# Optimization experiments

Measured on AMD Instinct MI355X. Metric: run time of the kernel, lower is better.

The kernel has to match this reference:

```python
import jax, jax.numpy as jnp
import numpy as np

N = 4096      # n_nodes
IN = 256      # in_features
H = 4         # n_heads
F = 64        # out_features (per head)
SLOPE = 0.2   # leaky relu negative slope


def setup_inputs() -> dict:
    key = jax.random.key(0)
    k0, k1, k2, k3 = jax.random.split(key, 4)
    h = jax.random.normal(k0, (N, IN), dtype=jnp.float32)
    adj = jax.random.randint(k1, (N, N), 0, 2, dtype=jnp.int32)
    # ensure every node has at least one neighbor (self-loop) so softmax is defined
    adj = jnp.maximum(adj, jnp.eye(N, dtype=jnp.int32))
    # linear: in_features -> out_features * n_heads (xavier-ish scale)
    W = jax.random.normal(k2, (H * F, IN), dtype=jnp.float32) * np.float32(1.0 / np.sqrt(IN))
    b = jnp.zeros((H * F,), dtype=jnp.float32)
    # attn: Linear(2*F -> 1), weight row vector of size 2F plus scalar bias
    attn_w = jax.random.normal(k3, (2 * F,), dtype=jnp.float32) * np.float32(1.0 / np.sqrt(2 * F))
    attn_b = jnp.zeros((1,), dtype=jnp.float32)
    return {"h": h, "adj_mat": adj, "W": W, "b": b, "attn_w": attn_w, "attn_b": attn_b}


def reference(h, adj_mat, W, b, attn_w, attn_b):
    n = h.shape[0]
    # node projection: [N, H, F]
    g = (h @ W.T + b).reshape(n, H, F)
    # attn(concat(h_i, h_j)) = <a_src, g_i> + <a_dst, g_j> + bias  (decomposed, same math)
    src = jnp.einsum('nhf,f->nh', g, attn_w[:F])   # [N, H] contribution of node i
    dst = jnp.einsum('nhf,f->nh', g, attn_w[F:])   # [N, H] contribution of node j
    e = src[:, None, :] + dst[None, :, :] + attn_b[0]   # [N, N, H]
    e = jnp.where(e >= 0, e, SLOPE * e)                 # leaky relu
    e = jnp.where(adj_mat[:, :, None] != 0, e, -jnp.inf)  # mask non-edges
    a = jax.nn.softmax(e, axis=1)                       # softmax over neighbors j
    out = jnp.einsum('ijh,jhf->ihf', a, g)              # [N, H, F]
    return out.mean(axis=1)                             # average heads -> [N, F]
```

## Files before the change

kernel.cpp:

```cpp
#include <hip/hip_runtime.h>
#include <stdint.h>

constexpr int NODES = 4096;
constexpr int KIN   = 256;
constexpr int NHEAD = 4;
constexpr int NF    = 64;
constexpr int HFQ   = 256;
#define SLOPE 0.2f
#define L2E 1.44269504088896340736f

typedef __attribute__((ext_vector_type(8))) short short8;
typedef __attribute__((ext_vector_type(4))) float floatx4;
typedef __attribute__((ext_vector_type(16))) float f32x16;

static __device__ __forceinline__ unsigned short f2bf(float f) {
  return __builtin_bit_cast(unsigned short, (__bf16)f);
}

__global__ __launch_bounds__(256) void pack_prep_kernel(
    const int* __restrict__ adj, unsigned* __restrict__ bm,
    const float* __restrict__ hin, const float* __restrict__ Win,
    unsigned short* __restrict__ hB, unsigned short* __restrict__ WB) {
  int tid = threadIdx.x;
  if (blockIdx.x < 2048) {
    int wv = blockIdx.x * 4 + (tid >> 6);
    int lane = tid & 63;
    int jw = wv & 127;
    int it = wv >> 7;
    int i = it * 64 + lane;
    const int4* p = reinterpret_cast<const int4*>(adj + (size_t)i * NODES + jw * 32);
    unsigned m = 0;
#pragma unroll
    for (int q = 0; q < 8; ++q) {
      int4 a = p[q];
      m |= (a.x != 0 ? 1u : 0u) << (q * 4);
      m |= (a.y != 0 ? 1u : 0u) << (q * 4 + 1);
      m |= (a.z != 0 ? 1u : 0u) << (q * 4 + 2);
      m |= (a.w != 0 ? 1u : 0u) << (q * 4 + 3);
    }
    bm[(size_t)jw * NODES + i] = m;
  } else {
    int idx = (blockIdx.x - 2048) * 256 + tid;
    const int NH4 = (NODES * KIN) / 4;
    const int NW4 = (HFQ * KIN) / 4;
    if (idx < NH4) {
      float4 v = reinterpret_cast<const float4*>(hin)[idx];
      ushort4 o = { f2bf(v.x), f2bf(v.y), f2bf(v.z), f2bf(v.w) };
      reinterpret_cast<ushort4*>(hB)[idx] = o;
    } else if (idx < NH4 + NW4) {
      int j = idx - NH4;
      float4 v = reinterpret_cast<const float4*>(Win)[j];
      ushort4 o = { f2bf(v.x), f2bf(v.y), f2bf(v.z), f2bf(v.w) };
      reinterpret_cast<ushort4*>(WB)[j] = o;
    }
  }
}

__global__ __launch_bounds__(256) void proj_kernel(
    const unsigned short* __restrict__ hB, const unsigned short* __restrict__ WB,
    const float* __restrict__ bias,
    float* __restrict__ g32, unsigned short* __restrict__ gT3) {
  int wave = threadIdx.x >> 6, lane = threadIdx.x & 63;
  int tile = blockIdx.x * 4 + wave;
  int mt = tile >> 4, nt = tile & 15;
  int m0 = mt * 16, n0 = nt * 16;
  int r = lane & 15, kg = lane >> 4;
  floatx4 acc = {0.f, 0.f, 0.f, 0.f};
  const short8* Ap = reinterpret_cast<const short8*>(hB + (m0 + r) * KIN + kg * 8);
  const short8* Bp = reinterpret_cast<const short8*>(WB + (n0 + r) * KIN + kg * 8);
#pragma unroll
  for (int kb = 0; kb < 8; ++kb) {
    short8 a = Ap[kb * 4];
    short8 b = Bp[kb * 4];
    acc = __builtin_amdgcn_mfma_f32_16x16x32_bf16(a, b, acc, 0, 0, 0);
  }
  int col = n0 + r;
  float bv = bias[col];
  int head = col >> 6, half = (col >> 5) & 1, il = col & 31;
#pragma unroll
  for (int q = 0; q < 4; ++q) {
    int row = m0 + kg * 4 + q;
    float v = acc[q] + bv;
    g32[row * HFQ + col] = v;
    int si = (row >> 5) * 8192 + head * 2048 + half * 1024 +
             ((row >> 4) & 1) * 512 + ((row >> 3) & 1) * 256 + il * 8 + (row & 7);
    gT3[si] = f2bf(v);
  }
}

__global__ __launch_bounds__(256) void srcdst_kernel(
    const float* __restrict__ g32, const float* __restrict__ attn_w,
    const float* __restrict__ attn_b,
    float4* __restrict__ srcP, unsigned* __restrict__ eP) {
  int wave = threadIdx.x >> 6, lane = threadIdx.x & 63;
  int n = blockIdx.x * 4 + wave;
  float aws = attn_w[lane], awd = attn_w[64 + lane];
  float ab = attn_b[0];
#pragma unroll
  for (int hh = 0; hh < NHEAD; ++hh) {
    float v = g32[n * HFQ + hh * NF + lane];
    float s = v * aws, d = v * awd;
#pragma unroll
    for (int m = 32; m >= 1; m >>= 1) {
      s += __shfl_xor(s, m, 64);
      d += __shfl_xor(d, m, 64);
    }
    if (lane == 0) {
      s += ab;
      float4 sp;
      sp.x = exp2f(s * L2E);
      sp.y = exp2f(0.2f * s * L2E);
      sp.z = exp2f(-s * L2E);
      sp.w = 0.f;
      srcP[n * NHEAD + hh] = sp;
      float e1 = exp2f(d * L2E), e2 = exp2f(0.2f * d * L2E);
      eP[hh * NODES + n] = ((unsigned)f2bf(e2) << 16) | (unsigned)f2bf(e1);
    }
  }
}

__global__ __launch_bounds__(256, 4) void attn_kernel(
    const unsigned* __restrict__ bm, const unsigned short* __restrict__ gT3,
    const float4* __restrict__ srcP, const unsigned* __restrict__ eP,
    float* __restrict__ pnum, float* __restrict__ pden, int JP) {
  int tid = threadIdx.x;
  int hh = tid >> 6, lane = tid & 63;
  int il = lane & 31, hi = lane >> 5;
  int part = blockIdx.x, itile = blockIdx.y;
  int jstart = part * JP;
  int i = itile * 32 + il;

  float4 sp = srcP[i * NHEAD + hh];
  float es1 = sp.x, es2 = sp.y, thr = sp.z;

  f32x16 acc0 = {0.f,0.f,0.f,0.f,0.f,0.f,0.f,0.f,0.f,0.f,0.f,0.f,0.f,0.f,0.f,0.f};
  f32x16 acc1 = acc0, accd = acc0;

  short8 ones;
#pragma unroll
  for (int r = 0; r < 8; ++r) ones[r] = (short)0x3F80;

  const unsigned* epb = eP + hh * NODES;
  const unsigned short* Ab = gT3 + hh * 2048;

  int nsteps = JP / 32;
  for (int stp = 0; stp < nsteps; ++stp) {
    int j0 = jstart + stp * 32;
    unsigned mwd = bm[(size_t)(j0 >> 5) * NODES + i];
    const unsigned short* At = Ab + (size_t)(j0 >> 5) * 8192;
#pragma unroll
    for (int ch = 0; ch < 2; ++ch) {
      int jc = j0 + ch * 16 + hi * 8;
      uint4 ea = *reinterpret_cast<const uint4*>(epb + jc);
      uint4 eb = *reinterpret_cast<const uint4*>(epb + jc + 4);
      unsigned mb = (mwd >> (ch * 16 + hi * 8)) & 0xFFu;
      unsigned ev[8] = {ea.x, ea.y, ea.z, ea.w, eb.x, eb.y, eb.z, eb.w};
      short8 bfr;
#pragma unroll
      for (int r = 0; r < 8; ++r) {
        float e1f = __builtin_bit_cast(float, ev[r] << 16);
        float e2f = __builtin_bit_cast(float, ev[r] & 0xFFFF0000u);
        bool sel = e1f >= thr;
        float w = (sel ? es1 : es2) * (sel ? e1f : e2f);
        w = (mb & (1u << r)) ? w : 0.f;
        bfr[r] = (short)f2bf(w);
      }
      const short8 a0 = *reinterpret_cast<const short8*>(At + ch * 512 + hi * 256 + il * 8);
      const short8 a1 = *reinterpret_cast<const short8*>(At + 1024 + ch * 512 + hi * 256 + il * 8);
      acc0 = __builtin_amdgcn_mfma_f32_32x32x16_bf16(a0, bfr, acc0, 0, 0, 0);
      acc1 = __builtin_amdgcn_mfma_f32_32x32x16_bf16(a1, bfr, acc1, 0, 0, 0);
      accd = __builtin_amdgcn_mfma_f32_32x32x16_bf16(ones, bfr, accd, 0, 0, 0);
    }
  }

  if (hi == 0)
    pden[(size_t)part * (NODES * NHEAD) + i * NHEAD + hh] = accd[0];

  float* pbase = pnum + (size_t)part * (NODES * HFQ) + (size_t)i * HFQ + hh * NF;
#pragma unroll
  for (int reg = 0; reg < 16; ++reg) {
    int crow = (reg & 3) + 8 * (reg >> 2) + 4 * hi;
    pbase[crow] = acc0[reg];
    pbase[32 + crow] = acc1[reg];
  }
}

__global__ __launch_bounds__(256) void combine_kernel(
    const float* __restrict__ pnum, const float* __restrict__ pden,
    float* __restrict__ out, int NP) {
  int idx = blockIdx.x * 256 + threadIdx.x;
  int i = idx >> 6, f = idx & 63;
  float o = 0.f;
#pragma unroll
  for (int hh = 0; hh < NHEAD; ++hh) {
    float num = 0.f, den = 0.f;
    for (int p = 0; p < NP; ++p) {
      num += pnum[p * (NODES * HFQ) + i * HFQ + hh * NF + f];
      den += pden[p * (NODES * NHEAD) + i * NHEAD + hh];
    }
    o += num / den;
  }
  out[idx] = 0.25f * o;
}

extern "C" void kernel_launch(void* const* d_in, const int* in_sizes, int n_in,
                              void* d_out, int out_size, void* d_ws, size_t ws_size,
                              hipStream_t stream) {
  const float* hin = (const float*)d_in[0];
  const int* adj   = (const int*)d_in[1];
  const float* W   = (const float*)d_in[2];
  const float* b   = (const float*)d_in[3];
  const float* aw  = (const float*)d_in[4];
  const float* ab  = (const float*)d_in[5];
  float* out = (float*)d_out;
  char* ws = (char*)d_ws;

  unsigned short* hB  = (unsigned short*)(ws + 0x000000);
  unsigned short* WB  = (unsigned short*)(ws + 0x200000);
  float* g32          = (float*)(ws + 0x400000);
  unsigned short* gT3 = (unsigned short*)(ws + 0x800000);
  float4* srcP        = (float4*)(ws + 0xA00000);
  unsigned* eP        = (unsigned*)(ws + 0xA40000);
  unsigned* bm        = (unsigned*)(ws + 0xA60000);
  float* pden         = (float*)(ws + 0xC60000);
  float* pnum         = (float*)(ws + 0xD00000);
  const size_t base = 0xD00000;

  int NP = 2;
  if (ws_size >= base + 8ull * NODES * HFQ * 4) NP = 8;
  else if (ws_size >= base + 4ull * NODES * HFQ * 4) NP = 4;
  int JP = NODES / NP;

  pack_prep_kernel<<<2048 + 1088, 256, 0, stream>>>(adj, bm, hin, W, hB, WB);
  proj_kernel<<<1024, 256, 0, stream>>>(hB, WB, b, g32, gT3);
  srcdst_kernel<<<1024, 256, 0, stream>>>(g32, aw, ab, srcP, eP);
  attn_kernel<<<dim3(NP, 128), 256, 0, stream>>>(bm, gT3, srcP, eP, pnum, pden, JP);
  combine_kernel<<<1024, 256, 0, stream>>>(pnum, pden, out, NP);
}
```

Baseline: 82.18 us.

## Switch attention aggregation to 16x16x32 MFMA tiles with 16-node row tiles

The attention kernel now uses 16x16x32 bf16 MFMAs over 16 destination nodes per block instead of 32x32x16 over 32 nodes. The grid doubles along the node axis and the launch bound allows 8 blocks per CU. The projection kernel's bf16 transposed-g layout is rearranged to match the new fragment layout. The aim is higher occupancy and more parallel blocks through smaller accumulators. In exchange, each block recomputes the per-edge weight work for fewer outputs, the ones-vector denominator MFMA is a larger share of the work, and the bf16 g tiles are reloaded by twice as many blocks.

```diff
diff --git a/kernel.cpp b/kernel.cpp
--- a/kernel.cpp
+++ b/kernel.cpp
@@ -11,7 +11,6 @@
 
 typedef __attribute__((ext_vector_type(8))) short short8;
 typedef __attribute__((ext_vector_type(4))) float floatx4;
-typedef __attribute__((ext_vector_type(16))) float f32x16;
 
 static __device__ __forceinline__ unsigned short f2bf(float f) {
   return __builtin_bit_cast(unsigned short, (__bf16)f);
@@ -76,14 +75,14 @@
   }
   int col = n0 + r;
   float bv = bias[col];
-  int head = col >> 6, half = (col >> 5) & 1, il = col & 31;
+  int head = col >> 6, ct = (col & 63) >> 4, c15 = col & 15;
 #pragma unroll
   for (int q = 0; q < 4; ++q) {
     int row = m0 + kg * 4 + q;
     float v = acc[q] + bv;
     g32[row * HFQ + col] = v;
-    int si = (row >> 5) * 8192 + head * 2048 + half * 1024 +
-             ((row >> 4) & 1) * 512 + ((row >> 3) & 1) * 256 + il * 8 + (row & 7);
+    int si = (row >> 5) * 8192 + head * 2048 + ct * 512 +
+             (((row >> 3) & 3) * 16 + c15) * 8 + (row & 7);
     gT3[si] = f2bf(v);
   }
 }
@@ -119,22 +118,22 @@
   }
 }
 
-__global__ __launch_bounds__(256, 4) void attn_kernel(
+__global__ __launch_bounds__(256, 8) void attn_kernel(
     const unsigned* __restrict__ bm, const unsigned short* __restrict__ gT3,
     const float4* __restrict__ srcP, const unsigned* __restrict__ eP,
     float* __restrict__ pnum, float* __restrict__ pden, int JP) {
   int tid = threadIdx.x;
   int hh = tid >> 6, lane = tid & 63;
-  int il = lane & 31, hi = lane >> 5;
+  int il = lane & 15, kg = lane >> 4;
   int part = blockIdx.x, itile = blockIdx.y;
   int jstart = part * JP;
-  int i = itile * 32 + il;
+  int i = itile * 16 + il;
 
   float4 sp = srcP[i * NHEAD + hh];
   float es1 = sp.x, es2 = sp.y, thr = sp.z;
 
-  f32x16 acc0 = {0.f,0.f,0.f,0.f,0.f,0.f,0.f,0.f,0.f,0.f,0.f,0.f,0.f,0.f,0.f,0.f};
-  f32x16 acc1 = acc0, accd = acc0;
+  floatx4 acc0 = {0.f, 0.f, 0.f, 0.f};
+  floatx4 acc1 = acc0, acc2 = acc0, acc3 = acc0, accd = acc0;
 
   short8 ones;
 #pragma unroll
@@ -146,42 +145,46 @@
   int nsteps = JP / 32;
   for (int stp = 0; stp < nsteps; ++stp) {
     int j0 = jstart + stp * 32;
-    unsigned mwd = bm[(size_t)(j0 >> 5) * NODES + i];
-    const unsigned short* At = Ab + (size_t)(j0 >> 5) * 8192;
-#pragma unroll
-    for (int ch = 0; ch < 2; ++ch) {
-      int jc = j0 + ch * 16 + hi * 8;
-      uint4 ea = *reinterpret_cast<const uint4*>(epb + jc);
-      uint4 eb = *reinterpret_cast<const uint4*>(epb + jc + 4);
-      unsigned mb = (mwd >> (ch * 16 + hi * 8)) & 0xFFu;
-      unsigned ev[8] = {ea.x, ea.y, ea.z, ea.w, eb.x, eb.y, eb.z, eb.w};
-      short8 bfr;
-#pragma unroll
-      for (int r = 0; r < 8; ++r) {
-        float e1f = __builtin_bit_cast(float, ev[r] << 16);
-        float e2f = __builtin_bit_cast(float, ev[r] & 0xFFFF0000u);
-        bool sel = e1f >= thr;
-        float w = (sel ? es1 : es2) * (sel ? e1f : e2f);
-        w = (mb & (1u << r)) ? w : 0.f;
-        bfr[r] = (short)f2bf(w);
-      }
-      const short8 a0 = *reinterpret_cast<const short8*>(At + ch * 512 + hi * 256 + il * 8);
-      const short8 a1 = *reinterpret_cast<const short8*>(At + 1024 + ch * 512 + hi * 256 + il * 8);
-      acc0 = __builtin_amdgcn_mfma_f32_32x32x16_bf16(a0, bfr, acc0, 0, 0, 0);
-      acc1 = __builtin_amdgcn_mfma_f32_32x32x16_bf16(a1, bfr, acc1, 0, 0, 0);
-      accd = __builtin_amdgcn_mfma_f32_32x32x16_bf16(ones, bfr, accd, 0, 0, 0);
-    }
-  }
-
-  if (hi == 0)
+    int jt = j0 >> 5;
+    unsigned mwd = bm[(size_t)jt * NODES + i];
+    unsigned mb = (mwd >> (kg * 8)) & 0xFFu;
+    const unsigned* ep = epb + j0 + kg * 8;
+    uint4 ea = *reinterpret_cast<const uint4*>(ep);
+    uint4 eb = *reinterpret_cast<const uint4*>(ep + 4);
+    unsigned ev[8] = {ea.x, ea.y, ea.z, ea.w, eb.x, eb.y, eb.z, eb.w};
+    short8 bfr;
+#pragma unroll
+    for (int r = 0; r < 8; ++r) {
+      float e1f = __builtin_bit_cast(float, ev[r] << 16);
+      float e2f = __builtin_bit_cast(float, ev[r] & 0xFFFF0000u);
+      bool sel = e1f >= thr;
+      float w = (sel ? es1 : es2) * (sel ? e1f : e2f);
+      w = (mb & (1u << r)) ? w : 0.f;
+      bfr[r] = (short)f2bf(w);
+    }
+    const unsigned short* At = Ab + (size_t)jt * 8192;
+    const short8 a0 = *reinterpret_cast<const short8*>(At + 0 * 512 + lane * 8);
+    const short8 a1 = *reinterpret_cast<const short8*>(At + 1 * 512 + lane * 8);
+    const short8 a2 = *reinterpret_cast<const short8*>(At + 2 * 512 + lane * 8);
+    const short8 a3 = *reinterpret_cast<const short8*>(At + 3 * 512 + lane * 8);
+    acc0 = __builtin_amdgcn_mfma_f32_16x16x32_bf16(a0, bfr, acc0, 0, 0, 0);
+    acc1 = __builtin_amdgcn_mfma_f32_16x16x32_bf16(a1, bfr, acc1, 0, 0, 0);
+    acc2 = __builtin_amdgcn_mfma_f32_16x16x32_bf16(a2, bfr, acc2, 0, 0, 0);
+    acc3 = __builtin_amdgcn_mfma_f32_16x16x32_bf16(a3, bfr, acc3, 0, 0, 0);
+    accd = __builtin_amdgcn_mfma_f32_16x16x32_bf16(ones, bfr, accd, 0, 0, 0);
+  }
+
+  if (kg == 0)
     pden[(size_t)part * (NODES * NHEAD) + i * NHEAD + hh] = accd[0];
 
   float* pbase = pnum + (size_t)part * (NODES * HFQ) + (size_t)i * HFQ + hh * NF;
 #pragma unroll
-  for (int reg = 0; reg < 16; ++reg) {
-    int crow = (reg & 3) + 8 * (reg >> 2) + 4 * hi;
-    pbase[crow] = acc0[reg];
-    pbase[32 + crow] = acc1[reg];
+  for (int q = 0; q < 4; ++q) {
+    int c = kg * 4 + q;
+    pbase[c] = acc0[q];
+    pbase[16 + c] = acc1[q];
+    pbase[32 + c] = acc2[q];
+    pbase[48 + c] = acc3[q];
   }
 }
 
@@ -234,6 +237,6 @@
   pack_prep_kernel<<<2048 + 1088, 256, 0, stream>>>(adj, bm, hin, W, hB, WB);
   proj_kernel<<<1024, 256, 0, stream>>>(hB, WB, b, g32, gT3);
   srcdst_kernel<<<1024, 256, 0, stream>>>(g32, aw, ab, srcP, eP);
-  attn_kernel<<<dim3(NP, 128), 256, 0, stream>>>(bm, gT3, srcP, eP, pnum, pden, JP);
+  attn_kernel<<<dim3(NP, 256), 256, 0, stream>>>(bm, gT3, srcP, eP, pnum, pden, JP);
   combine_kernel<<<1024, 256, 0, stream>>>(pnum, pden, out, NP);
 }
```

New measurement: 80.93 us. Within noise of the previous version (-1.5%).
